# Kernel optimization log

Measured on AMD Instinct MI355X. Metric: run time of the kernel, lower is better.

Reference implementation:

```python
import jax, jax.numpy as jnp
import numpy as np

USER_NUM = 100000
ITEM_NUM = 50000
REC_DIM = 64
N_LAYERS = 3
N_EDGES = 2400000
N_NODES = USER_NUM + ITEM_NUM
BATCH = 4096


def setup_inputs() -> dict:
    key = jax.random.key(0)
    ks = jax.random.split(key, 7)
    user_emb = jax.random.normal(ks[0], (USER_NUM, REC_DIM), dtype=jnp.float32) * 0.1
    item_emb = jax.random.normal(ks[1], (ITEM_NUM, REC_DIM), dtype=jnp.float32) * 0.1
    edge_src = jax.random.randint(ks[2], (N_EDGES,), 0, N_NODES, dtype=jnp.int32)
    edge_dst = jax.random.randint(ks[3], (N_EDGES,), 0, N_NODES, dtype=jnp.int32)
    # symmetric-normalized adjacency values (positive)
    edge_val = jax.random.uniform(ks[4], (N_EDGES,), dtype=jnp.float32)
    users = jax.random.randint(ks[5], (BATCH,), 0, USER_NUM, dtype=jnp.int32)
    items = jax.random.randint(ks[6], (BATCH,), 0, ITEM_NUM, dtype=jnp.int32)
    return {"user_emb": user_emb, "item_emb": item_emb, "edge_src": edge_src,
            "edge_dst": edge_dst, "edge_val": edge_val, "users": users, "items": items}


def _spmm(edge_src, edge_dst, edge_val, emb):
    # out[d] = sum_{e: dst(e)=d} val(e) * emb[src(e)]   (sparse adjacency @ emb)
    msgs = edge_val[:, None] * emb[edge_src]  # [E, d]
    return jax.ops.segment_sum(msgs, edge_dst, num_segments=N_NODES)


def _propagate(user_emb, item_emb, edge_src, edge_dst, edge_val):
    e = jnp.concatenate([user_emb, item_emb], axis=0)  # [N, d]
    acc = e  # running sum instead of stack+mean
    for _ in range(N_LAYERS):
        e = _spmm(edge_src, edge_dst, edge_val, e)
        acc = acc + e
    mean = acc / float(N_LAYERS + 1)
    return mean[:USER_NUM], mean[USER_NUM:]


def reference(user_emb, item_emb, edge_src, edge_dst, edge_val, users, items):
    all_users, all_items = _propagate(user_emb, item_emb, edge_src, edge_dst, edge_val)
    users_emb = all_users[users]  # [B, d]
    items_emb = all_items[items]  # [B, d]
    gamma = jnp.sum(users_emb * items_emb, axis=1)
    return jax.nn.sigmoid(gamma)
```

## Files before the change

kernel.cpp:

```cpp
#include <hip/hip_runtime.h>
#include <hip/hip_bf16.h>
#include <hip/hip_fp16.h>

#define USER_NUM 100000
#define ITEM_NUM 50000
#define NNODES   150000
#define DIM      64
#define NEDGES   2400000
#define BATCH    4096

#define SPN      1024
#define NSUP     ((NNODES + SPN - 1) / SPN)
#define NSUPP    160
#define CHUNK    4096
#define NBLK     ((NEDGES + CHUNK - 1) / CHUNK)

__device__ inline float4 h4_to_f4(float2 raw) {
    __half2 a = ((__half2*)&raw)[0];
    __half2 b = ((__half2*)&raw)[1];
    float2 fa = __half22float2(a);
    float2 fb = __half22float2(b);
    return make_float4(fa.x, fa.y, fb.x, fb.y);
}

__device__ inline float2 f4_to_h4(float4 s) {
    __half2 a = __floats2half2_rn(s.x, s.y);
    __half2 b = __floats2half2_rn(s.z, s.w);
    float2 st;
    ((__half2*)&st)[0] = a;
    ((__half2*)&st)[1] = b;
    return st;
}

__global__ void init_kernel(const float* __restrict__ user_emb,
                            const float* __restrict__ item_emb,
                            __half* __restrict__ curh) {
    const long total4 = (long)NNODES * DIM / 4;
    long i = (long)blockIdx.x * blockDim.x + threadIdx.x;
    if (i >= total4) return;
    const long user4 = (long)USER_NUM * DIM / 4;
    float4 v;
    if (i < user4) v = ((const float4*)user_emb)[i];
    else           v = ((const float4*)item_emb)[i - user4];
    ((float2*)curh)[i] = f4_to_h4(v);
}

__global__ void sample_init_kernel(const float* __restrict__ user_emb,
                                   const float* __restrict__ item_emb,
                                   const int* __restrict__ users,
                                   const int* __restrict__ items,
                                   float* __restrict__ acc_s) {
    int t = blockIdx.x * blockDim.x + threadIdx.x;
    int slot = t >> 4;
    if (slot >= 2 * BATCH) return;
    int k = (t & 15) * 4;
    const float* src = (slot < BATCH)
        ? &user_emb[(long)users[slot] * DIM]
        : &item_emb[(long)items[slot - BATCH] * DIM];
    *(float4*)&acc_s[(long)slot * DIM + k] = *(const float4*)&src[k];
}

__global__ void sample_add_kernel(const __half* __restrict__ tab,
                                  const int* __restrict__ users,
                                  const int* __restrict__ items,
                                  float* __restrict__ acc_s) {
    int t = blockIdx.x * blockDim.x + threadIdx.x;
    int slot = t >> 4;
    if (slot >= 2 * BATCH) return;
    int k = (t & 15) * 4;
    int node = (slot < BATCH) ? users[slot] : USER_NUM + items[slot - BATCH];
    float4 x = h4_to_f4(*(const float2*)&tab[(long)node * DIM + k]);
    long o = (long)slot * DIM + k;
    float4 a = *(float4*)&acc_s[o];
    a.x += x.x; a.y += x.y; a.z += x.z; a.w += x.w;
    *(float4*)&acc_s[o] = a;
}

__global__ void bucket_hist_kernel(const int* __restrict__ edge_dst,
                                   int* __restrict__ bucket_cnt,
                                   int* __restrict__ blockhist) {
    __shared__ int h[NSUP];
    for (int t = threadIdx.x; t < NSUP; t += blockDim.x) h[t] = 0;
    __syncthreads();
    int lo = blockIdx.x * CHUNK;
    int hi = min(lo + CHUNK, NEDGES);
    for (int j = lo + (int)threadIdx.x; j < hi; j += blockDim.x)
        atomicAdd(&h[edge_dst[j] >> 10], 1);
    __syncthreads();
    for (int t = threadIdx.x; t < NSUP; t += blockDim.x) {
        int c = h[t];
        blockhist[blockIdx.x * NSUPP + t] = c;
        if (c) atomicAdd(&bucket_cnt[t], c);
    }
}

__global__ void bucket_scan_kernel(const int* __restrict__ bucket_cnt,
                                   int* __restrict__ bucket_base,
                                   int* __restrict__ fill,
                                   int* __restrict__ row_ptr) {
    __shared__ int s[256];
    int tid = threadIdx.x;
    int v = (tid < NSUP) ? bucket_cnt[tid] : 0;
    s[tid] = v;
    __syncthreads();
    for (int off = 1; off < 256; off <<= 1) {
        int t = (tid >= off) ? s[tid - off] : 0;
        __syncthreads();
        s[tid] += t;
        __syncthreads();
    }
    if (tid < NSUP) {
        int excl = s[tid] - v;
        bucket_base[tid] = excl;
        fill[tid] = excl;
    }
    if (tid == 0) {
        bucket_base[NSUP] = NEDGES;
        row_ptr[NNODES] = NEDGES;
    }
}

__global__ __launch_bounds__(256) void partition_kernel(
        const int* __restrict__ edge_src,
        const int* __restrict__ edge_dst,
        const float* __restrict__ edge_val,
        const int* __restrict__ blockhist,
        int* __restrict__ fill,
        int2* __restrict__ tmp) {
    __shared__ int cur_[NSUP];
    __shared__ int goff[NSUP];
    __shared__ int sc[256];
    __shared__ unsigned char sbkt[CHUNK];
    __shared__ int2 sout[CHUNK];
    int tid = threadIdx.x;
    int lo = blockIdx.x * CHUNK;
    int hi = min(lo + CHUNK, NEDGES);
    int n = hi - lo;

    int c = (tid < NSUP) ? blockhist[blockIdx.x * NSUPP + tid] : 0;
    sc[tid] = c;
    __syncthreads();
    for (int off = 1; off < 256; off <<= 1) {
        int t = (tid >= off) ? sc[tid - off] : 0;
        __syncthreads();
        sc[tid] += t;
        __syncthreads();
    }
    if (tid < NSUP) {
        int excl = sc[tid] - c;
        cur_[tid] = excl;
        goff[tid] = (c ? atomicAdd(&fill[tid], c) : 0) - excl;
    }
    __syncthreads();
    for (int i = tid; i < n; i += 256) {
        int d = edge_dst[lo + i];
        int b = d >> 10;
        int pos = atomicAdd(&cur_[b], 1);
        sout[pos] = make_int2(__float_as_int(edge_val[lo + i]),
                              edge_src[lo + i] | ((d & (SPN - 1)) << 18));
        sbkt[pos] = (unsigned char)b;
    }
    __syncthreads();
    for (int i = tid; i < n; i += 256) {
        int b = sbkt[i];
        tmp[goff[b] + i] = sout[i];
    }
}

__global__ __launch_bounds__(1024) void local_sort_kernel(
        const int* __restrict__ bucket_base,
        const int2* __restrict__ tmp,
        int* __restrict__ row_ptr,
        int2* __restrict__ sedge) {
    __shared__ int h[SPN];
    __shared__ int sc[SPN];
    __shared__ int cur[SPN];
    int b = blockIdx.x;
    int base = bucket_base[b];
    int end  = bucket_base[b + 1];
    int tid = threadIdx.x;
    h[tid] = 0;
    __syncthreads();
    for (int j = base + tid; j < end; j += 1024)
        atomicAdd(&h[(tmp[j].y >> 18) & (SPN - 1)], 1);
    __syncthreads();
    int c = h[tid];
    sc[tid] = c;
    __syncthreads();
    for (int off = 1; off < SPN; off <<= 1) {
        int t = (tid >= off) ? sc[tid - off] : 0;
        __syncthreads();
        sc[tid] += t;
        __syncthreads();
    }
    int excl = sc[tid] - c;
    cur[tid] = base + excl;
    int node = b * SPN + tid;
    if (node < NNODES) row_ptr[node] = base + excl;
    __syncthreads();
    for (int j = base + tid; j < end; j += 1024) {
        int2 e = tmp[j];
        int dl = (e.y >> 18) & (SPN - 1);
        int pos = atomicAdd(&cur[dl], 1);
        sedge[pos] = make_int2(e.y & 0x3FFFF, e.x);
    }
}

__global__ void spmm_kernel(const int* __restrict__ row_ptr,
                            const int2* __restrict__ sedge,
                            const __half* __restrict__ cur,
                            __half* __restrict__ next) {
    long t = (long)blockIdx.x * blockDim.x + threadIdx.x;
    int row = (int)(t >> 3);
    if (row >= NNODES) return;
    int k = ((int)t & 7) * 8;
    int start = row_ptr[row];
    int end   = row_ptr[row + 1];
    float a0[8], a1[8], a2[8], a3[8];
    #pragma unroll
    for (int q = 0; q < 8; ++q) { a0[q] = 0.f; a1[q] = 0.f; a2[q] = 0.f; a3[q] = 0.f; }
    int j = start;
    for (; j + 4 <= end; j += 4) {
        int2 e0 = sedge[j];
        int2 e1 = sedge[j + 1];
        int2 e2 = sedge[j + 2];
        int2 e3 = sedge[j + 3];
        float4 r0 = *(const float4*)&cur[(long)e0.x * DIM + k];
        float4 r1 = *(const float4*)&cur[(long)e1.x * DIM + k];
        float4 r2 = *(const float4*)&cur[(long)e2.x * DIM + k];
        float4 r3 = *(const float4*)&cur[(long)e3.x * DIM + k];
        float v0 = __int_as_float(e0.y), v1 = __int_as_float(e1.y);
        float v2 = __int_as_float(e2.y), v3 = __int_as_float(e3.y);
        const __half2* h0 = (const __half2*)&r0;
        const __half2* h1 = (const __half2*)&r1;
        const __half2* h2 = (const __half2*)&r2;
        const __half2* h3 = (const __half2*)&r3;
        #pragma unroll
        for (int q = 0; q < 4; ++q) {
            float2 f0 = __half22float2(h0[q]);
            float2 f1 = __half22float2(h1[q]);
            float2 f2 = __half22float2(h2[q]);
            float2 f3 = __half22float2(h3[q]);
            a0[2*q]   += v0 * f0.x;  a0[2*q+1] += v0 * f0.y;
            a1[2*q]   += v1 * f1.x;  a1[2*q+1] += v1 * f1.y;
            a2[2*q]   += v2 * f2.x;  a2[2*q+1] += v2 * f2.y;
            a3[2*q]   += v3 * f3.x;  a3[2*q+1] += v3 * f3.y;
        }
    }
    for (; j < end; ++j) {
        int2 e = sedge[j];
        float v = __int_as_float(e.y);
        float4 r = *(const float4*)&cur[(long)e.x * DIM + k];
        const __half2* h = (const __half2*)&r;
        #pragma unroll
        for (int q = 0; q < 4; ++q) {
            float2 f = __half22float2(h[q]);
            a0[2*q]   += v * f.x;
            a0[2*q+1] += v * f.y;
        }
    }
    float4 st;
    __half2* sh = (__half2*)&st;
    #pragma unroll
    for (int q = 0; q < 4; ++q) {
        float lo = (a0[2*q]   + a1[2*q])   + (a2[2*q]   + a3[2*q]);
        float hi = (a0[2*q+1] + a1[2*q+1]) + (a2[2*q+1] + a3[2*q+1]);
        sh[q] = __floats2half2_rn(lo, hi);
    }
    *(float4*)&next[(long)row * DIM + k] = st;
}

__global__ void spmm_sampled_kernel(const int* __restrict__ row_ptr,
                                    const int2* __restrict__ sedge,
                                    const __half* __restrict__ cur,
                                    const int* __restrict__ users,
                                    const int* __restrict__ items,
                                    float* __restrict__ acc_s) {
    int t = blockIdx.x * blockDim.x + threadIdx.x;
    int slot = t >> 4;
    if (slot >= 2 * BATCH) return;
    int k = (t & 15) * 4;
    int node = (slot < BATCH) ? users[slot] : USER_NUM + items[slot - BATCH];
    int start = row_ptr[node];
    int end   = row_ptr[node + 1];
    float4 s0 = make_float4(0.f, 0.f, 0.f, 0.f);
    float4 s1 = s0, s2 = s0, s3 = s0;
    int j = start;
    for (; j + 4 <= end; j += 4) {
        int2 e0 = sedge[j];
        int2 e1 = sedge[j + 1];
        int2 e2 = sedge[j + 2];
        int2 e3 = sedge[j + 3];
        float4 x0 = h4_to_f4(*(const float2*)&cur[(long)e0.x * DIM + k]);
        float4 x1 = h4_to_f4(*(const float2*)&cur[(long)e1.x * DIM + k]);
        float4 x2 = h4_to_f4(*(const float2*)&cur[(long)e2.x * DIM + k]);
        float4 x3 = h4_to_f4(*(const float2*)&cur[(long)e3.x * DIM + k]);
        float v0 = __int_as_float(e0.y), v1 = __int_as_float(e1.y);
        float v2 = __int_as_float(e2.y), v3 = __int_as_float(e3.y);
        s0.x += v0 * x0.x; s0.y += v0 * x0.y; s0.z += v0 * x0.z; s0.w += v0 * x0.w;
        s1.x += v1 * x1.x; s1.y += v1 * x1.y; s1.z += v1 * x1.z; s1.w += v1 * x1.w;
        s2.x += v2 * x2.x; s2.y += v2 * x2.y; s2.z += v2 * x2.z; s2.w += v2 * x2.w;
        s3.x += v3 * x3.x; s3.y += v3 * x3.y; s3.z += v3 * x3.z; s3.w += v3 * x3.w;
    }
    for (; j < end; ++j) {
        int2 e = sedge[j];
        float v = __int_as_float(e.y);
        float4 x = h4_to_f4(*(const float2*)&cur[(long)e.x * DIM + k]);
        s0.x += v * x.x; s0.y += v * x.y; s0.z += v * x.z; s0.w += v * x.w;
    }
    long o = (long)slot * DIM + k;
    float4 a = *(float4*)&acc_s[o];
    a.x += (s0.x + s1.x) + (s2.x + s3.x);
    a.y += (s0.y + s1.y) + (s2.y + s3.y);
    a.z += (s0.z + s1.z) + (s2.z + s3.z);
    a.w += (s0.w + s1.w) + (s2.w + s3.w);
    *(float4*)&acc_s[o] = a;
}

__global__ void dot_kernel(const float* __restrict__ acc_s,
                           float* __restrict__ out) {
    int w = (int)(((long)blockIdx.x * blockDim.x + threadIdx.x) >> 6);
    int lane = threadIdx.x & 63;
    if (w >= BATCH) return;
    float a = acc_s[(long)w * DIM + lane];
    float b = acc_s[(long)(BATCH + w) * DIM + lane];
    float p = a * b;
    #pragma unroll
    for (int off = 32; off; off >>= 1) p += __shfl_down(p, off);
    if (lane == 0) {
        float gamma = p * (1.0f / 16.0f);
        out[w] = 1.0f / (1.0f + __expf(-gamma));
    }
}

extern "C" void kernel_launch(void* const* d_in, const int* in_sizes, int n_in,
                              void* d_out, int out_size, void* d_ws, size_t ws_size,
                              hipStream_t stream) {
    const float* user_emb = (const float*)d_in[0];
    const float* item_emb = (const float*)d_in[1];
    const int*   edge_src = (const int*)d_in[2];
    const int*   edge_dst = (const int*)d_in[3];
    const float* edge_val = (const float*)d_in[4];
    const int*   users    = (const int*)d_in[5];
    const int*   items    = (const int*)d_in[6];
    float* out = (float*)d_out;

    const size_t tbl  = (size_t)NNODES * DIM * sizeof(float);
    const size_t htbl = (size_t)NNODES * DIM * sizeof(__half);
    char* w = (char*)d_ws;
    float*  acc_s       = (float*)w;   w += tbl;
    char*   bufA        = w;           w += tbl;
    char*   bufB        = w;           w += tbl;
    int2*   sedge       = (int2*)w;    w += (size_t)NEDGES * 8;
    int*    row_ptr     = (int*)w;     w += ((size_t)NNODES + 16) * 4;
    int*    bucket_cnt  = (int*)w;     w += ((size_t)NSUP + 8) * 4;
    int*    bucket_base = (int*)w;     w += ((size_t)NSUP + 8) * 4;
    int*    fill        = (int*)w;     w += ((size_t)NSUP + 8) * 4;
    int*    blockhist   = (int*)w;     w += (size_t)NBLK * NSUPP * 4;

    int2*   tmp   = (int2*)bufA;
    __half* tabA  = (__half*)bufB;
    __half* tabB  = (__half*)(bufB + htbl);

    hipMemsetAsync(bucket_cnt, 0, (size_t)NSUP * 4, stream);
    bucket_hist_kernel<<<NBLK, 256, 0, stream>>>(edge_dst, bucket_cnt, blockhist);
    bucket_scan_kernel<<<1, 256, 0, stream>>>(bucket_cnt, bucket_base, fill, row_ptr);
    partition_kernel<<<NBLK, 256, 0, stream>>>(edge_src, edge_dst, edge_val,
                                               blockhist, fill, tmp);
    local_sort_kernel<<<NSUP, 1024, 0, stream>>>(bucket_base, tmp, row_ptr, sedge);

    {
        long total4 = (long)NNODES * DIM / 4;
        init_kernel<<<(unsigned)((total4 + 255) / 256), 256, 0, stream>>>(
            user_emb, item_emb, tabA);
    }
    const unsigned samp_grid = (2 * BATCH * 16 + 255) / 256;
    sample_init_kernel<<<samp_grid, 256, 0, stream>>>(user_emb, item_emb,
                                                      users, items, acc_s);

    const unsigned spmm_grid = (unsigned)(((long)NNODES * 8 + 255) / 256);
    spmm_kernel<<<spmm_grid, 256, 0, stream>>>(row_ptr, sedge, tabA, tabB);
    sample_add_kernel<<<samp_grid, 256, 0, stream>>>(tabB, users, items, acc_s);
    spmm_kernel<<<spmm_grid, 256, 0, stream>>>(row_ptr, sedge, tabB, tabA);
    sample_add_kernel<<<samp_grid, 256, 0, stream>>>(tabA, users, items, acc_s);
    spmm_sampled_kernel<<<samp_grid, 256, 0, stream>>>(row_ptr, sedge, tabA,
                                                       users, items, acc_s);
    dot_kernel<<<(BATCH * 64 + 255) / 256, 256, 0, stream>>>(acc_s, out);
}
```

Measured before the change: 219.3 us.

## Merge small kernels into combined launches and fuse final layer with dot

Folds the bucket histogram, fp16 table init and sampled-row init into one combined grid. The sample-add of layer 1 is merged into the second SpMM launch as extra blocks, and the layer-2 sample-add, sampled third-layer SpMM and the dot/sigmoid are fused into one pair kernel that exchanges user and item halves with warp shuffles. This removes several launch and serialization gaps. In exchange, independent work now shares grids with different block roles, and the final kernel uses two accumulators instead of four.

```diff
diff --git a/kernel.cpp b/kernel.cpp
--- a/kernel.cpp
+++ b/kernel.cpp
@@ -14,6 +14,9 @@
 #define NSUPP    160
 #define CHUNK    4096
 #define NBLK     ((NEDGES + CHUNK - 1) / CHUNK)
+#define INIT_B   ((NNODES * DIM / 4 + 255) / 256)
+#define SAMP_B   ((2 * BATCH * 16 + 255) / 256)
+#define SPMM_B   ((NNODES * 8 + 255) / 256)
 
 __device__ inline float4 h4_to_f4(float2 raw) {
     __half2 a = ((__half2*)&raw)[0];
@@ -32,65 +35,49 @@
     return st;
 }
 
-__global__ void init_kernel(const float* __restrict__ user_emb,
-                            const float* __restrict__ item_emb,
-                            __half* __restrict__ curh) {
-    const long total4 = (long)NNODES * DIM / 4;
-    long i = (long)blockIdx.x * blockDim.x + threadIdx.x;
-    if (i >= total4) return;
-    const long user4 = (long)USER_NUM * DIM / 4;
-    float4 v;
-    if (i < user4) v = ((const float4*)user_emb)[i];
-    else           v = ((const float4*)item_emb)[i - user4];
-    ((float2*)curh)[i] = f4_to_h4(v);
-}
-
-__global__ void sample_init_kernel(const float* __restrict__ user_emb,
-                                   const float* __restrict__ item_emb,
-                                   const int* __restrict__ users,
-                                   const int* __restrict__ items,
-                                   float* __restrict__ acc_s) {
-    int t = blockIdx.x * blockDim.x + threadIdx.x;
-    int slot = t >> 4;
-    if (slot >= 2 * BATCH) return;
-    int k = (t & 15) * 4;
-    const float* src = (slot < BATCH)
-        ? &user_emb[(long)users[slot] * DIM]
-        : &item_emb[(long)items[slot - BATCH] * DIM];
-    *(float4*)&acc_s[(long)slot * DIM + k] = *(const float4*)&src[k];
-}
-
-__global__ void sample_add_kernel(const __half* __restrict__ tab,
-                                  const int* __restrict__ users,
-                                  const int* __restrict__ items,
-                                  float* __restrict__ acc_s) {
-    int t = blockIdx.x * blockDim.x + threadIdx.x;
-    int slot = t >> 4;
-    if (slot >= 2 * BATCH) return;
-    int k = (t & 15) * 4;
-    int node = (slot < BATCH) ? users[slot] : USER_NUM + items[slot - BATCH];
-    float4 x = h4_to_f4(*(const float2*)&tab[(long)node * DIM + k]);
-    long o = (long)slot * DIM + k;
-    float4 a = *(float4*)&acc_s[o];
-    a.x += x.x; a.y += x.y; a.z += x.z; a.w += x.w;
-    *(float4*)&acc_s[o] = a;
-}
-
-__global__ void bucket_hist_kernel(const int* __restrict__ edge_dst,
-                                   int* __restrict__ bucket_cnt,
-                                   int* __restrict__ blockhist) {
+__global__ __launch_bounds__(256) void mega1_kernel(
+        const int* __restrict__ edge_dst,
+        int* __restrict__ bucket_cnt,
+        int* __restrict__ blockhist,
+        const float* __restrict__ user_emb,
+        const float* __restrict__ item_emb,
+        __half* __restrict__ curh,
+        const int* __restrict__ users,
+        const int* __restrict__ items,
+        float* __restrict__ acc_s) {
     __shared__ int h[NSUP];
-    for (int t = threadIdx.x; t < NSUP; t += blockDim.x) h[t] = 0;
-    __syncthreads();
-    int lo = blockIdx.x * CHUNK;
-    int hi = min(lo + CHUNK, NEDGES);
-    for (int j = lo + (int)threadIdx.x; j < hi; j += blockDim.x)
-        atomicAdd(&h[edge_dst[j] >> 10], 1);
-    __syncthreads();
-    for (int t = threadIdx.x; t < NSUP; t += blockDim.x) {
-        int c = h[t];
-        blockhist[blockIdx.x * NSUPP + t] = c;
-        if (c) atomicAdd(&bucket_cnt[t], c);
+    int b = blockIdx.x;
+    if (b < NBLK) {
+        for (int t = threadIdx.x; t < NSUP; t += blockDim.x) h[t] = 0;
+        __syncthreads();
+        int lo = b * CHUNK;
+        int hi = min(lo + CHUNK, NEDGES);
+        for (int j = lo + (int)threadIdx.x; j < hi; j += blockDim.x)
+            atomicAdd(&h[edge_dst[j] >> 10], 1);
+        __syncthreads();
+        for (int t = threadIdx.x; t < NSUP; t += blockDim.x) {
+            int c = h[t];
+            blockhist[b * NSUPP + t] = c;
+            if (c) atomicAdd(&bucket_cnt[t], c);
+        }
+    } else if (b < NBLK + INIT_B) {
+        const long total4 = (long)NNODES * DIM / 4;
+        long i = (long)(b - NBLK) * 256 + threadIdx.x;
+        if (i >= total4) return;
+        const long user4 = (long)USER_NUM * DIM / 4;
+        float4 v;
+        if (i < user4) v = ((const float4*)user_emb)[i];
+        else           v = ((const float4*)item_emb)[i - user4];
+        ((float2*)curh)[i] = f4_to_h4(v);
+    } else {
+        int t = (b - NBLK - INIT_B) * 256 + threadIdx.x;
+        int slot = t >> 4;
+        if (slot >= 2 * BATCH) return;
+        int k = (t & 15) * 4;
+        const float* src = (slot < BATCH)
+            ? &user_emb[(long)users[slot] * DIM]
+            : &item_emb[(long)items[slot - BATCH] * DIM];
+        *(float4*)&acc_s[(long)slot * DIM + k] = *(const float4*)&src[k];
     }
 }
 
@@ -206,11 +193,11 @@
     }
 }
 
-__global__ void spmm_kernel(const int* __restrict__ row_ptr,
-                            const int2* __restrict__ sedge,
-                            const __half* __restrict__ cur,
-                            __half* __restrict__ next) {
-    long t = (long)blockIdx.x * blockDim.x + threadIdx.x;
+__device__ inline void spmm_body(int gblock, const int* __restrict__ row_ptr,
+                                 const int2* __restrict__ sedge,
+                                 const __half* __restrict__ cur,
+                                 __half* __restrict__ next) {
+    long t = (long)gblock * 256 + threadIdx.x;
     int row = (int)(t >> 3);
     if (row >= NNODES) return;
     int k = ((int)t & 7) * 8;
@@ -270,66 +257,92 @@
     *(float4*)&next[(long)row * DIM + k] = st;
 }
 
-__global__ void spmm_sampled_kernel(const int* __restrict__ row_ptr,
-                                    const int2* __restrict__ sedge,
-                                    const __half* __restrict__ cur,
-                                    const int* __restrict__ users,
-                                    const int* __restrict__ items,
-                                    float* __restrict__ acc_s) {
-    int t = blockIdx.x * blockDim.x + threadIdx.x;
-    int slot = t >> 4;
-    if (slot >= 2 * BATCH) return;
-    int k = (t & 15) * 4;
-    int node = (slot < BATCH) ? users[slot] : USER_NUM + items[slot - BATCH];
+__global__ void spmm_kernel(const int* __restrict__ row_ptr,
+                            const int2* __restrict__ sedge,
+                            const __half* __restrict__ cur,
+                            __half* __restrict__ next) {
+    spmm_body(blockIdx.x, row_ptr, sedge, cur, next);
+}
+
+__global__ void spmm_sa_kernel(const int* __restrict__ row_ptr,
+                               const int2* __restrict__ sedge,
+                               const __half* __restrict__ cur,
+                               __half* __restrict__ next,
+                               const int* __restrict__ users,
+                               const int* __restrict__ items,
+                               float* __restrict__ acc_s) {
+    if (blockIdx.x < SPMM_B) {
+        spmm_body(blockIdx.x, row_ptr, sedge, cur, next);
+    } else {
+        int t = (blockIdx.x - SPMM_B) * 256 + threadIdx.x;
+        int slot = t >> 4;
+        if (slot >= 2 * BATCH) return;
+        int k = (t & 15) * 4;
+        int node = (slot < BATCH) ? users[slot] : USER_NUM + items[slot - BATCH];
+        float4 x = h4_to_f4(*(const float2*)&cur[(long)node * DIM + k]);
+        long o = (long)slot * DIM + k;
+        float4 a = *(float4*)&acc_s[o];
+        a.x += x.x; a.y += x.y; a.z += x.z; a.w += x.w;
+        *(float4*)&acc_s[o] = a;
+    }
+}
+
+__global__ __launch_bounds__(256) void pair_kernel(
+        const int* __restrict__ row_ptr,
+        const int2* __restrict__ sedge,
+        const __half* __restrict__ tab,
+        const int* __restrict__ users,
+        const int* __restrict__ items,
+        const float* __restrict__ acc_s,
+        float* __restrict__ out) {
+    int t = blockIdx.x * 256 + threadIdx.x;
+    int p = t >> 5;
+    if (p >= BATCH) return;
+    int sub = t & 31;
+    int lane = threadIdx.x & 63;
+    bool isU = (sub < 16);
+    int k = (sub & 15) * 4;
+    int node = isU ? users[p] : USER_NUM + items[p];
+    int slot = isU ? p : BATCH + p;
+
     int start = row_ptr[node];
     int end   = row_ptr[node + 1];
     float4 s0 = make_float4(0.f, 0.f, 0.f, 0.f);
-    float4 s1 = s0, s2 = s0, s3 = s0;
+    float4 s1 = s0;
     int j = start;
-    for (; j + 4 <= end; j += 4) {
+    for (; j + 2 <= end; j += 2) {
         int2 e0 = sedge[j];
         int2 e1 = sedge[j + 1];
-        int2 e2 = sedge[j + 2];
-        int2 e3 = sedge[j + 3];
-        float4 x0 = h4_to_f4(*(const float2*)&cur[(long)e0.x * DIM + k]);
-        float4 x1 = h4_to_f4(*(const float2*)&cur[(long)e1.x * DIM + k]);
-        float4 x2 = h4_to_f4(*(const float2*)&cur[(long)e2.x * DIM + k]);
-        float4 x3 = h4_to_f4(*(const float2*)&cur[(long)e3.x * DIM + k]);
+        float4 x0 = h4_to_f4(*(const float2*)&tab[(long)e0.x * DIM + k]);
+        float4 x1 = h4_to_f4(*(const float2*)&tab[(long)e1.x * DIM + k]);
         float v0 = __int_as_float(e0.y), v1 = __int_as_float(e1.y);
-        float v2 = __int_as_float(e2.y), v3 = __int_as_float(e3.y);
         s0.x += v0 * x0.x; s0.y += v0 * x0.y; s0.z += v0 * x0.z; s0.w += v0 * x0.w;
         s1.x += v1 * x1.x; s1.y += v1 * x1.y; s1.z += v1 * x1.z; s1.w += v1 * x1.w;
-        s2.x += v2 * x2.x; s2.y += v2 * x2.y; s2.z += v2 * x2.z; s2.w += v2 * x2.w;
-        s3.x += v3 * x3.x; s3.y += v3 * x3.y; s3.z += v3 * x3.z; s3.w += v3 * x3.w;
     }
     for (; j < end; ++j) {
         int2 e = sedge[j];
         float v = __int_as_float(e.y);
-        float4 x = h4_to_f4(*(const float2*)&cur[(long)e.x * DIM + k]);
+        float4 x = h4_to_f4(*(const float2*)&tab[(long)e.x * DIM + k]);
         s0.x += v * x.x; s0.y += v * x.y; s0.z += v * x.z; s0.w += v * x.w;
     }
-    long o = (long)slot * DIM + k;
-    float4 a = *(float4*)&acc_s[o];
-    a.x += (s0.x + s1.x) + (s2.x + s3.x);
-    a.y += (s0.y + s1.y) + (s2.y + s3.y);
-    a.z += (s0.z + s1.z) + (s2.z + s3.z);
-    a.w += (s0.w + s1.w) + (s2.w + s3.w);
-    *(float4*)&acc_s[o] = a;
-}
-
-__global__ void dot_kernel(const float* __restrict__ acc_s,
-                           float* __restrict__ out) {
-    int w = (int)(((long)blockIdx.x * blockDim.x + threadIdx.x) >> 6);
-    int lane = threadIdx.x & 63;
-    if (w >= BATCH) return;
-    float a = acc_s[(long)w * DIM + lane];
-    float b = acc_s[(long)(BATCH + w) * DIM + lane];
-    float p = a * b;
+    float4 a = *(const float4*)&acc_s[(long)slot * DIM + k];
+    float4 e2v = h4_to_f4(*(const float2*)&tab[(long)node * DIM + k]);
+    a.x += e2v.x + s0.x + s1.x;
+    a.y += e2v.y + s0.y + s1.y;
+    a.z += e2v.z + s0.z + s1.z;
+    a.w += e2v.w + s0.w + s1.w;
+
+    int partner = (lane + 16) & 63;
+    float bx = __shfl(a.x, partner);
+    float by = __shfl(a.y, partner);
+    float bz = __shfl(a.z, partner);
+    float bw = __shfl(a.w, partner);
+    float pd = a.x * bx + a.y * by + a.z * bz + a.w * bw;
     #pragma unroll
-    for (int off = 32; off; off >>= 1) p += __shfl_down(p, off);
-    if (lane == 0) {
-        float gamma = p * (1.0f / 16.0f);
-        out[w] = 1.0f / (1.0f + __expf(-gamma));
+    for (int off = 1; off < 16; off <<= 1) pd += __shfl_xor(pd, off);
+    if (sub == 0) {
+        float gamma = pd * (1.0f / 16.0f);
+        out[p] = 1.0f / (1.0f + __expf(-gamma));
     }
 }
 
@@ -363,27 +376,18 @@
     __half* tabB  = (__half*)(bufB + htbl);
 
     hipMemsetAsync(bucket_cnt, 0, (size_t)NSUP * 4, stream);
-    bucket_hist_kernel<<<NBLK, 256, 0, stream>>>(edge_dst, bucket_cnt, blockhist);
+    mega1_kernel<<<NBLK + INIT_B + SAMP_B, 256, 0, stream>>>(
+        edge_dst, bucket_cnt, blockhist,
+        user_emb, item_emb, tabA, users, items, acc_s);
+
     bucket_scan_kernel<<<1, 256, 0, stream>>>(bucket_cnt, bucket_base, fill, row_ptr);
     partition_kernel<<<NBLK, 256, 0, stream>>>(edge_src, edge_dst, edge_val,
                                                blockhist, fill, tmp);
     local_sort_kernel<<<NSUP, 1024, 0, stream>>>(bucket_base, tmp, row_ptr, sedge);
 
-    {
-        long total4 = (long)NNODES * DIM / 4;
-        init_kernel<<<(unsigned)((total4 + 255) / 256), 256, 0, stream>>>(
-            user_emb, item_emb, tabA);
-    }
-    const unsigned samp_grid = (2 * BATCH * 16 + 255) / 256;
-    sample_init_kernel<<<samp_grid, 256, 0, stream>>>(user_emb, item_emb,
-                                                      users, items, acc_s);
-
-    const unsigned spmm_grid = (unsigned)(((long)NNODES * 8 + 255) / 256);
-    spmm_kernel<<<spmm_grid, 256, 0, stream>>>(row_ptr, sedge, tabA, tabB);
-    sample_add_kernel<<<samp_grid, 256, 0, stream>>>(tabB, users, items, acc_s);
-    spmm_kernel<<<spmm_grid, 256, 0, stream>>>(row_ptr, sedge, tabB, tabA);
-    sample_add_kernel<<<samp_grid, 256, 0, stream>>>(tabA, users, items, acc_s);
-    spmm_sampled_kernel<<<samp_grid, 256, 0, stream>>>(row_ptr, sedge, tabA,
-                                                       users, items, acc_s);
-    dot_kernel<<<(BATCH * 64 + 255) / 256, 256, 0, stream>>>(acc_s, out);
-}
+    spmm_kernel<<<SPMM_B, 256, 0, stream>>>(row_ptr, sedge, tabA, tabB);
+    spmm_sa_kernel<<<SPMM_B + SAMP_B, 256, 0, stream>>>(row_ptr, sedge, tabB, tabA,
+                                                        users, items, acc_s);
+    pair_kernel<<<(BATCH * 32 + 255) / 256, 256, 0, stream>>>(
+        row_ptr, sedge, tabA, users, items, acc_s, out);
+}
```

New measurement: 206.9 us. -5.6%, faster.
